# Kernel tuning notes

Hardware: AMD Instinct MI355X
Metric: run time of the kernel (lower is better)

Reference implementation:

```python
import jax, jax.numpy as jnp
import numpy as np
import math

H = 16
D_ATTN = 64
D_MID = 64
D_X = 1024
D_Z = 1024
D_OUT = 1024
B = 2
L_X = 2048
L_Z = 2048
MINUS_INFINITY = -1000000.0

def _xavier(key, shape):
    fan_in, fan_out = shape
    limit = math.sqrt(6.0 / (fan_in + fan_out))
    return jax.random.uniform(key, shape, jnp.float32, -limit, limit)

def setup_inputs() -> dict:
    key = jax.random.key(0)
    ks = jax.random.split(key, 8)
    primary = jax.random.normal(ks[0], (B, L_X, D_X), jnp.float32)
    context = jax.random.normal(ks[1], (B, L_Z, D_Z), jnp.float32)
    padding_mask = jnp.ones((B, L_Z), jnp.int32)
    # causal attention mask (b, l_x, l_z)
    attention_mask = jnp.broadcast_to(
        jnp.tril(jnp.ones((L_X, L_Z), jnp.int32))[None], (B, L_X, L_Z))
    W_qs = _xavier(ks[2], (D_X, H * D_ATTN))
    W_ks = _xavier(ks[3], (D_Z, H * D_ATTN))
    W_vs = _xavier(ks[4], (D_Z, H * D_MID))
    W_o = _xavier(ks[5], (H * D_MID, D_OUT))
    b_o = jnp.zeros((D_OUT,), jnp.float32)
    return {"primary": primary, "context": context,
            "padding_mask": padding_mask, "attention_mask": attention_mask,
            "W_qs": W_qs, "W_ks": W_ks, "W_vs": W_vs, "W_o": W_o, "b_o": b_o}

def reference(primary, context, padding_mask, attention_mask, W_qs, W_ks, W_vs, W_o, b_o):
    b, l_x, _ = primary.shape
    l_z = context.shape[1]
    # QKV projections, split into heads (head-major columns)
    q = (primary @ W_qs).reshape(b, l_x, H, D_ATTN).transpose(0, 2, 1, 3)  # (b,h,l_x,d_attn)
    k = (context @ W_ks).reshape(b, l_z, H, D_ATTN).transpose(0, 2, 1, 3)  # (b,h,l_z,d_attn)
    v = (context @ W_vs).reshape(b, l_z, H, D_MID).transpose(0, 2, 1, 3)   # (b,h,l_z,d_mid)
    scores = jnp.einsum('bhxd,bhzd->bhxz', q, k) / math.sqrt(D_ATTN)
    # combined mask: attention_mask AND padding_mask, broadcast over heads
    mask = (attention_mask * padding_mask[:, None, :])[:, None]  # (b,1,l_x,l_z)
    scores = jnp.where(mask == 0, MINUS_INFINITY, scores)
    attn = jax.nn.softmax(scores, axis=-1)
    out = jnp.einsum('bhxz,bhzm->bhxm', attn, v)  # (b,h,l_x,d_mid)
    out = out.transpose(0, 2, 1, 3).reshape(b, l_x, H * D_MID)
    return out @ W_o + b_o
```

## Files before the change

### kernel.cpp

```cpp
#include <hip/hip_runtime.h>

#define NB 2
#define LX 2048
#define LZ 2048
#define HH 16
#define DA 64
#define DM 64
#define HD 1024
#define KVS 2048
#define MINF  -1000000.0f
#define QSC   0.1803368801f
#define DTHR  8.0f

typedef __attribute__((ext_vector_type(8))) short short8;
typedef __attribute__((ext_vector_type(4))) float f32x4;

static __device__ __forceinline__ ushort f2bf(float f) {
    union { float f; uint32_t u; } c; c.f = f;
    return (ushort)((c.u + 0x7FFFu + ((c.u >> 16) & 1u)) >> 16);
}

static __device__ __forceinline__ float bf2f(ushort u) {
    union { uint32_t u; float f; } c; c.u = (uint32_t)u << 16;
    return c.f;
}

static __device__ __forceinline__ uint32_t cvtpk(float lo, float hi) {
    uint32_t r;
    asm("v_cvt_pk_bf16_f32 %0, %1, %2" : "=v"(r) : "v"(lo), "v"(hi));
    return r;
}

#define GL16(g, l) __builtin_amdgcn_global_load_lds( \
    (const __attribute__((address_space(1))) void*)(g), \
    (__attribute__((address_space(3))) void*)(l), 16, 0, 0)

__global__ __launch_bounds__(256) void prep(
    const float* __restrict__ pA, const float* __restrict__ pB,
    ushort* __restrict__ oA, ushort* __restrict__ oB,
    const float* __restrict__ W0, const float* __restrict__ W1,
    const float* __restrict__ W2, const float* __restrict__ W3,
    ushort* __restrict__ T0, ushort* __restrict__ T1,
    ushort* __restrict__ T2, ushort* __restrict__ T3,
    const int* __restrict__ amask, const int* __restrict__ pmask,
    int* __restrict__ cls)
{
    const int fid = blockIdx.x;
    const int t = threadIdx.x;
    if (fid < 8192) {
        const int i = fid * 256 + t;
        const float* in = (i < 1048576) ? pA : pB;
        ushort* out = (i < 1048576) ? oA : oB;
        const int j = i & 1048575;
        float4 v = ((const float4*)in)[j];
        ushort4 o;
        o.x = f2bf(v.x); o.y = f2bf(v.y); o.z = f2bf(v.z); o.w = f2bf(v.w);
        ((ushort4*)out)[j] = o;
    } else if (fid < 9216) {
        __shared__ ushort Ls[64][72];
        const int id2 = fid - 8192;
        const int zz = id2 >> 8, rem = id2 & 255;
        const float* W = (zz == 0) ? W0 : (zz == 1) ? W1 : (zz == 2) ? W2 : W3;
        ushort* Wt = (zz == 0) ? T0 : (zz == 1) ? T1 : (zz == 2) ? T2 : T3;
        const int n0 = (rem & 15) * 64, k0 = (rem >> 4) * 64;
        const int rr = t >> 4, c4 = (t & 15) * 4;
        #pragma unroll
        for (int i = 0; i < 4; ++i) {
            const int r = rr + i * 16;
            float4 v = *(const float4*)&W[(size_t)(k0 + r) * 1024 + n0 + c4];
            Ls[c4 + 0][r] = f2bf(v.x);
            Ls[c4 + 1][r] = f2bf(v.y);
            Ls[c4 + 2][r] = f2bf(v.z);
            Ls[c4 + 3][r] = f2bf(v.w);
        }
        __syncthreads();
        const int n = t >> 2, kc = (t & 3) * 16;
        *(short8*)&Wt[(size_t)(n0 + n) * 1024 + k0 + kc]     = *(const short8*)&Ls[n][kc];
        *(short8*)&Wt[(size_t)(n0 + n) * 1024 + k0 + kc + 8] = *(const short8*)&Ls[n][kc + 8];
    } else {
        const int bid = fid - 9216;
        const int b = bid >> 10, xb = (bid >> 5) & 31, zb = bid & 31;
        int andv = 1, orv = 0;
        #pragma unroll
        for (int i = 0; i < 16; ++i) {
            const int e = t + i * 256;
            const int r = e >> 6, z = e & 63;
            const int m = amask[((size_t)b * LX + xb * 64 + r) * LZ + zb * 64 + z];
            const int p = pmask[(size_t)b * LZ + zb * 64 + z];
            const int v = (m != 0) & (p != 0);
            andv &= v; orv |= v;
        }
        __shared__ int sa[256];
        __shared__ int so[256];
        sa[t] = andv; so[t] = orv;
        __syncthreads();
        for (int s = 128; s > 0; s >>= 1) {
            if (t < s) { sa[t] &= sa[t + s]; so[t] |= so[t + s]; }
            __syncthreads();
        }
        if (t == 0) cls[bid] = so[0] ? (sa[0] ? 1 : 2) : 0;
    }
}

__global__ __launch_bounds__(256) void gemm_qkv(
    const ushort* __restrict__ Pb, const ushort* __restrict__ Cb,
    const ushort* __restrict__ Wqt, const ushort* __restrict__ Wkvt,
    ushort* __restrict__ Qb, ushort* __restrict__ KV)
{
    const int bx = blockIdx.x;
    const bool isQ = bx < 8;
    const ushort* A  = isQ ? Pb : Cb;
    const ushort* Bt = isQ ? Wqt : Wkvt;
    ushort* Cout = isQ ? Qb : KV;
    const int n0 = (isQ ? bx : bx - 8) * 128;
    const int ostr = isQ ? 1024 : KVS;
    const float osc = isQ ? QSC : 1.0f;

    __shared__ ushort As[128 * 32];
    __shared__ ushort Bs[128 * 32];
    const int t = threadIdx.x;
    const int w = t >> 6, l = t & 63, lr = l & 15, lg = l >> 4;
    const int wr = w >> 1, wc = w & 1;
    const int m0 = blockIdx.y * 128;

    const int c0 = t, c1 = t + 256;
    const ushort* a0 = &A[(size_t)(m0 + (c0 >> 2)) * 1024 + (c0 & 3) * 8];
    const ushort* a1 = &A[(size_t)(m0 + (c1 >> 2)) * 1024 + (c1 & 3) * 8];
    const ushort* b0 = &Bt[(size_t)(n0 + (c0 >> 2)) * 1024 + (c0 & 3) * 8];
    const ushort* b1 = &Bt[(size_t)(n0 + (c1 >> 2)) * 1024 + (c1 & 3) * 8];
    ushort* lA0 = &As[w * 512];
    ushort* lA1 = &As[(4 + w) * 512];
    ushort* lB0 = &Bs[w * 512];
    ushort* lB1 = &Bs[(4 + w) * 512];

    f32x4 acc[4][4];
    #pragma unroll
    for (int i = 0; i < 4; ++i)
        #pragma unroll
        for (int j = 0; j < 4; ++j) acc[i][j] = 0.f;

    for (int k0 = 0; k0 < 1024; k0 += 32) {
        __syncthreads();
        GL16(a0 + k0, lA0);
        GL16(a1 + k0, lA1);
        GL16(b0 + k0, lB0);
        GL16(b1 + k0, lB1);
        __syncthreads();
        short8 af[4], bf[4];
        #pragma unroll
        for (int mi = 0; mi < 4; ++mi)
            af[mi] = *(const short8*)&As[(wr * 64 + mi * 16 + lr) * 32 + lg * 8];
        #pragma unroll
        for (int nj = 0; nj < 4; ++nj)
            bf[nj] = *(const short8*)&Bs[(wc * 64 + nj * 16 + lr) * 32 + lg * 8];
        #pragma unroll
        for (int mi = 0; mi < 4; ++mi)
            #pragma unroll
            for (int nj = 0; nj < 4; ++nj)
                acc[mi][nj] = __builtin_amdgcn_mfma_f32_16x16x32_bf16(
                    af[mi], bf[nj], acc[mi][nj], 0, 0, 0);
    }

    const int row0 = m0 + wr * 64, col0 = n0 + wc * 64;
    #pragma unroll
    for (int mi = 0; mi < 4; ++mi)
        #pragma unroll
        for (int nj = 0; nj < 4; ++nj) {
            const int col = col0 + nj * 16 + lr;
            #pragma unroll
            for (int r = 0; r < 4; ++r) {
                const int row = row0 + mi * 16 + lg * 4 + r;
                Cout[(size_t)row * ostr + col] = f2bf(acc[mi][nj][r] * osc);
            }
        }
}

__global__ __launch_bounds__(256, 4) void attn_mfma(
    const ushort* __restrict__ Qg, const ushort* __restrict__ KVg,
    const int* __restrict__ amask, const int* __restrict__ pmask,
    const int* __restrict__ cls, ushort* __restrict__ Op,
    float2* __restrict__ ml)
{
    __shared__ ushort Ks[64 * 64];
    __shared__ ushort Vt[64 * 64];

    const int t = threadIdx.x, w = t >> 6, l = t & 63, lr = l & 15, lg = l >> 4;
    const int flat = blockIdx.x + 32 * (blockIdx.y + 16 * blockIdx.z);
    const int xcd = flat & 7, ii = flat >> 3;
    const int g = xcd + 8 * (ii >> 5);
    const int xr_ = ii & 31;
    const int h = g & 15, bs = g >> 4;
    const int b = bs & 1, sKV = bs >> 1;
    const int fx = (xr_ & 1) ? 31 - (xr_ >> 1) : (xr_ >> 1);
    const int qb = b ? 31 - fx : fx;
    const int qw = qb * 64 + w * 16;

    short8 qf[2];
    #pragma unroll
    for (int ks = 0; ks < 2; ++ks)
        qf[ks] = *(const short8*)&Qg[(size_t)(b * LX + qw + lr) * HD
                                     + h * DA + ks * 32 + lg * 8];

    float mrun = -1e30f, lrun = 0.f;
    f32x4 o[4];
    #pragma unroll
    for (int mj = 0; mj < 4; ++mj) o[mj] = 0.f;

    const int zs0 = t >> 3, zs1 = 32 + (t >> 3);
    const int cs = t & 7;
    const int gc0 = (cs ^ (zs0 & 7)) << 3;
    ushort* kdst0 = &Ks[w * 512];
    ushort* kdst1 = &Ks[2048 + w * 512];
    const size_t kbase = (size_t)(b * LZ) * KVS + h * DA;

    const int vz = (t >> 3) * 2, vc = (t & 7) * 8;

    for (int zb = sKV; zb < LZ / 64; zb += 2) {
        const int cl = cls[b * 1024 + qb * 32 + zb];
        if (cl == 0) continue;
        const int z0 = zb * 64;

        __syncthreads();
        GL16(&KVg[kbase + (size_t)(z0 + zs0) * KVS + gc0], kdst0);
        GL16(&KVg[kbase + (size_t)(z0 + zs1) * KVS + gc0], kdst1);
        {
            const ushort* vp = &KVg[(size_t)(b * LZ + z0 + vz) * KVS + 1024 + h * DM + vc];
            short8 v0 = *(const short8*)vp;
            short8 v1 = *(const short8*)(vp + KVS);
            const int zc = vz >> 3, zo = vz & 7;
            #pragma unroll
            for (int j = 0; j < 8; ++j) {
                const int m = vc + j;
                const int idx = m * 64 + (((zc ^ m ^ (m >> 3)) & 7) << 3) + zo;
                *(uint32_t*)&Vt[idx] =
                    (uint32_t)(ushort)v0[j] | ((uint32_t)(ushort)v1[j] << 16);
            }
        }
        __syncthreads();

        f32x4 s[4];
        __builtin_amdgcn_s_setprio(1);
        #pragma unroll
        for (int nj = 0; nj < 4; ++nj) {
            const int row = nj * 16 + lr;
            const int sw = row & 7;
            const short8 kf0 = *(const short8*)&Ks[row * 64 + ((lg ^ sw) << 3)];
            const short8 kf1 = *(const short8*)&Ks[row * 64 + (((4 + lg) ^ sw) << 3)];
            f32x4 z4 = 0.f;
            z4 = __builtin_amdgcn_mfma_f32_16x16x32_bf16(kf0, qf[0], z4, 0, 0, 0);
            z4 = __builtin_amdgcn_mfma_f32_16x16x32_bf16(kf1, qf[1], z4, 0, 0, 0);
            s[nj] = z4;
        }
        __builtin_amdgcn_s_setprio(0);
        if (cl == 2) {
            const size_t arow = (size_t)(b * LX + qw + lr) * LZ + z0;
            #pragma unroll
            for (int nj = 0; nj < 4; ++nj)
                #pragma unroll
                for (int r = 0; r < 4; ++r) {
                    const int z = nj * 16 + lg * 4 + r;
                    const int ok = (amask[arow + z] != 0) & (pmask[b * LZ + z0 + z] != 0);
                    if (!ok) s[nj][r] = MINF;
                }
        }
        {
            float pm = s[0][0];
            #pragma unroll
            for (int nj = 0; nj < 4; ++nj)
                #pragma unroll
                for (int r = 0; r < 4; ++r) pm = fmaxf(pm, s[nj][r]);
            pm = fmaxf(pm, __shfl_xor(pm, 16));
            pm = fmaxf(pm, __shfl_xor(pm, 32));
            if (__any(pm > mrun + DTHR)) {
                const float mn = fmaxf(mrun, pm);
                const float al = exp2f(mrun - mn);
                mrun = mn;
                lrun *= al;
                #pragma unroll
                for (int r = 0; r < 4; ++r) {
                    const float alq = __shfl(al, (lg << 2) + r);
                    #pragma unroll
                    for (int mj = 0; mj < 4; ++mj) o[mj][r] *= alq;
                }
            }
            #pragma unroll
            for (int nj = 0; nj < 4; ++nj)
                #pragma unroll
                for (int r = 0; r < 4; ++r) {
                    const float p = exp2f(s[nj][r] - mrun);
                    s[nj][r] = p;
                    lrun += p;
                }
        }
        short8 pa[2];
        {
            uint32_t pk01[4], pk23[4];
            #pragma unroll
            for (int nj = 0; nj < 4; ++nj) {
                pk01[nj] = cvtpk(s[nj][0], s[nj][1]);
                pk23[nj] = cvtpk(s[nj][2], s[nj][3]);
            }
            #pragma unroll
            for (int ks = 0; ks < 2; ++ks) {
                union { uint32_t d[4]; short8 v; } u;
                u.d[0] = pk01[2 * ks];
                u.d[1] = pk23[2 * ks];
                u.d[2] = pk01[2 * ks + 1];
                u.d[3] = pk23[2 * ks + 1];
                pa[ks] = u.v;
            }
        }
        __builtin_amdgcn_s_setprio(1);
        #pragma unroll
        for (int mj = 0; mj < 4; ++mj) {
            const int m_ = mj * 16 + lr;
            const int xr = (m_ ^ (m_ >> 3)) & 7;
            const int czb = lg >> 1;
            const int zo = (lg & 1) * 4;
            #pragma unroll
            for (int ks = 0; ks < 2; ++ks) {
                const int clo = (ks * 4 + czb) ^ xr;
                const int chi = (ks * 4 + 2 + czb) ^ xr;
                const uint2 lo = *(const uint2*)&Vt[m_ * 64 + ((clo & 7) << 3) + zo];
                const uint2 hi = *(const uint2*)&Vt[m_ * 64 + ((chi & 7) << 3) + zo];
                union { uint32_t d[4]; short8 v; } u;
                u.d[0] = lo.x; u.d[1] = lo.y; u.d[2] = hi.x; u.d[3] = hi.y;
                o[mj] = __builtin_amdgcn_mfma_f32_16x16x32_bf16(pa[ks], u.v, o[mj], 0, 0, 0);
            }
        }
        __builtin_amdgcn_s_setprio(0);
    }

    lrun += __shfl_xor(lrun, 16);
    lrun += __shfl_xor(lrun, 32);
    if (l < 16)
        ml[(size_t)((sKV * NB + b) * HH + h) * LX + qw + l] = make_float2(mrun, lrun);
    const size_t ob = (size_t)((sKV * NB + b) * LX + qw) * HD + h * DM;
    #pragma unroll
    for (int r = 0; r < 4; ++r)
        #pragma unroll
        for (int mj = 0; mj < 4; ++mj)
            Op[ob + (size_t)((lg << 2) + r) * HD + mj * 16 + lr] = f2bf(o[mj][r]);
}

__global__ __launch_bounds__(256) void gemm_out_fused(
    const ushort* __restrict__ Op, const float2* __restrict__ ml,
    const ushort* __restrict__ Bt, const float* __restrict__ bias,
    float* __restrict__ Cout)
{
    __shared__ ushort As[64 * 32];
    __shared__ ushort Bs[128 * 32];
    __shared__ float2 Wl[64][17];
    const int t = threadIdx.x;
    const int w = t >> 6, l = t & 63, lr = l & 15, lg = l >> 4;
    const int wr = w >> 1, wc = w & 1;
    const int n0 = blockIdx.x * 128, m0 = blockIdx.y * 64;

    {
        const int e = t * 4;
        #pragma unroll
        for (int j = 0; j < 4; ++j) {
            const int rl = (e + j) >> 4, hh = (e + j) & 15;
            const int ra = m0 + rl;
            const int bb = ra >> 11, xx = ra & 2047;
            const float2 a0 = ml[(size_t)(bb * HH + hh) * LX + xx];
            const float2 a1 = ml[(size_t)((NB + bb) * HH + hh) * LX + xx];
            const float M = fmaxf(a0.x, a1.x);
            const float w0 = exp2f(a0.x - M), w1 = exp2f(a1.x - M);
            const float inv = 1.f / fmaxf(a0.y * w0 + a1.y * w1, 1e-37f);
            Wl[rl][hh] = make_float2(w0 * inv, w1 * inv);
        }
    }
    __syncthreads();

    const int ra = m0 + (t >> 2), ka = (t & 3) * 8;
    const ushort* p0 = &Op[(size_t)ra * HD + ka];
    const ushort* p1 = p0 + (size_t)NB * LX * HD;
    const ushort* b0 = &Bt[(size_t)(n0 + (t >> 2)) * 1024 + ka];
    const ushort* b1 = &Bt[(size_t)(n0 + 64 + (t >> 2)) * 1024 + ka];
    ushort* lB0 = &Bs[w * 512];
    ushort* lB1 = &Bs[(4 + w) * 512];

    f32x4 acc[2][4];
    #pragma unroll
    for (int i = 0; i < 2; ++i)
        #pragma unroll
        for (int j = 0; j < 4; ++j) acc[i][j] = 0.f;

    for (int k0 = 0; k0 < 1024; k0 += 32) {
        const short8 q0 = *(const short8*)(p0 + k0);
        const short8 q1 = *(const short8*)(p1 + k0);
        const float2 wv = Wl[t >> 2][(k0 + ka) >> 6];
        union { ushort d[8]; short8 v; } av;
        #pragma unroll
        for (int j = 0; j < 8; ++j)
            av.d[j] = f2bf(bf2f((ushort)q0[j]) * wv.x + bf2f((ushort)q1[j]) * wv.y);
        __syncthreads();
        *(short8*)&As[t * 8] = av.v;
        GL16(b0 + k0, lB0);
        GL16(b1 + k0, lB1);
        __syncthreads();
        short8 af[2], bf[4];
        #pragma unroll
        for (int mi = 0; mi < 2; ++mi)
            af[mi] = *(const short8*)&As[(wr * 32 + mi * 16 + lr) * 32 + lg * 8];
        #pragma unroll
        for (int nj = 0; nj < 4; ++nj)
            bf[nj] = *(const short8*)&Bs[(wc * 64 + nj * 16 + lr) * 32 + lg * 8];
        #pragma unroll
        for (int mi = 0; mi < 2; ++mi)
            #pragma unroll
            for (int nj = 0; nj < 4; ++nj)
                acc[mi][nj] = __builtin_amdgcn_mfma_f32_16x16x32_bf16(
                    af[mi], bf[nj], acc[mi][nj], 0, 0, 0);
    }

    const int row0 = m0 + wr * 32, col0 = n0 + wc * 64;
    #pragma unroll
    for (int mi = 0; mi < 2; ++mi)
        #pragma unroll
        for (int nj = 0; nj < 4; ++nj) {
            const int col = col0 + nj * 16 + lr;
            #pragma unroll
            for (int r = 0; r < 4; ++r) {
                const int row = row0 + mi * 16 + lg * 4 + r;
                Cout[(size_t)row * 1024 + col] = acc[mi][nj][r] + bias[col];
            }
        }
}

extern "C" void kernel_launch(void* const* d_in, const int* in_sizes, int n_in,
                              void* d_out, int out_size, void* d_ws, size_t ws_size,
                              hipStream_t stream)
{
    const float* primary = (const float*)d_in[0];
    const float* context = (const float*)d_in[1];
    const int*   pmask   = (const int*)d_in[2];
    const int*   amask   = (const int*)d_in[3];
    const float* Wq      = (const float*)d_in[4];
    const float* Wk      = (const float*)d_in[5];
    const float* Wv      = (const float*)d_in[6];
    const float* Wo      = (const float*)d_in[7];
    const float* bo      = (const float*)d_in[8];
    float* out = (float*)d_out;

    char* w8 = (char*)d_ws;
    ushort* Pb  = (ushort*)(w8 + 0);
    ushort* Cb  = (ushort*)(w8 + 8388608);
    ushort* Qb  = (ushort*)(w8 + 16777216);
    ushort* KV  = (ushort*)(w8 + 25165824);
    ushort* Wqt = (ushort*)(w8 + 50331648);
    ushort* Wkt = (ushort*)(w8 + 52428800);
    ushort* Wvt = (ushort*)(w8 + 54525952);
    ushort* Wot = (ushort*)(w8 + 56623104);
    int*    clsp = (int*)(w8 + 58720256);
    ushort* Op   = Pb;
    float2* mlp  = (float2*)Wqt;

    prep<<<11264, 256, 0, stream>>>(primary, context, Pb, Cb,
                                    Wq, Wk, Wv, Wo, Wqt, Wkt, Wvt, Wot,
                                    amask, pmask, clsp);
    gemm_qkv<<<dim3(24, 32), 256, 0, stream>>>(Pb, Cb, Wqt, Wkt, Qb, KV);
    attn_mfma<<<dim3(32, 16, 4), 256, 0, stream>>>(Qb, KV, amask, pmask, clsp, Op, mlp);
    gemm_out_fused<<<dim3(8, 64), 256, 0, stream>>>(Op, mlp, Wot, bo, out);
}
```

Measured before the change: 137.0 us.

## Pair complementary causal query blocks per workgroup to share K/V tile loads

```diff
diff --git a/kernel.cpp b/kernel.cpp
--- a/kernel.cpp
+++ b/kernel.cpp
@@ -185,26 +185,36 @@
     __shared__ ushort Vt[64 * 64];
 
     const int t = threadIdx.x, w = t >> 6, l = t & 63, lr = l & 15, lg = l >> 4;
-    const int flat = blockIdx.x + 32 * (blockIdx.y + 16 * blockIdx.z);
+    const int flat = blockIdx.x + 16 * (blockIdx.y + 16 * blockIdx.z);
     const int xcd = flat & 7, ii = flat >> 3;
-    const int g = xcd + 8 * (ii >> 5);
-    const int xr_ = ii & 31;
+    const int g = xcd + 8 * (ii >> 4);
+    const int pp = ii & 15;
     const int h = g & 15, bs = g >> 4;
     const int b = bs & 1, sKV = bs >> 1;
-    const int fx = (xr_ & 1) ? 31 - (xr_ >> 1) : (xr_ >> 1);
-    const int qb = b ? 31 - fx : fx;
-    const int qw = qb * 64 + w * 16;
-
-    short8 qf[2];
-    #pragma unroll
-    for (int ks = 0; ks < 2; ++ks)
-        qf[ks] = *(const short8*)&Qg[(size_t)(b * LX + qw + lr) * HD
-                                     + h * DA + ks * 32 + lg * 8];
-
-    float mrun = -1e30f, lrun = 0.f;
-    f32x4 o[4];
-    #pragma unroll
-    for (int mj = 0; mj < 4; ++mj) o[mj] = 0.f;
+    const uint32_t halfm = sKV ? 0xAAAAAAAAu : 0x55555555u;
+
+    const int qb0 = pp, qb1 = 31 - pp;
+    const int qw0 = qb0 * 64 + w * 16, qw1 = qb1 * 64 + w * 16;
+    const int cv0 = cls[b * 1024 + qb0 * 32 + (l & 31)];
+    const int cv1 = cls[b * 1024 + qb1 * 32 + (l & 31)];
+    const uint32_t act0 = (uint32_t)__ballot(cv0 != 0) & halfm;
+    const uint32_t mix0 = (uint32_t)__ballot(cv0 == 2) & halfm;
+    const uint32_t act1 = (uint32_t)__ballot(cv1 != 0) & halfm;
+    const uint32_t mix1 = (uint32_t)__ballot(cv1 == 2) & halfm;
+
+    short8 qfA[2], qfB[2];
+    #pragma unroll
+    for (int ks = 0; ks < 2; ++ks) {
+        qfA[ks] = *(const short8*)&Qg[(size_t)(b * LX + qw0 + lr) * HD
+                                      + h * DA + ks * 32 + lg * 8];
+        qfB[ks] = *(const short8*)&Qg[(size_t)(b * LX + qw1 + lr) * HD
+                                      + h * DA + ks * 32 + lg * 8];
+    }
+
+    float mrunA = -1e30f, lrunA = 0.f, mrunB = -1e30f, lrunB = 0.f;
+    f32x4 oA[4], oB[4];
+    #pragma unroll
+    for (int mj = 0; mj < 4; ++mj) { oA[mj] = 0.f; oB[mj] = 0.f; }
 
     const int zs0 = t >> 3, zs1 = 32 + (t >> 3);
     const int cs = t & 7;
@@ -212,12 +222,107 @@
     ushort* kdst0 = &Ks[w * 512];
     ushort* kdst1 = &Ks[2048 + w * 512];
     const size_t kbase = (size_t)(b * LZ) * KVS + h * DA;
-
     const int vz = (t >> 3) * 2, vc = (t & 7) * 8;
 
-    for (int zb = sKV; zb < LZ / 64; zb += 2) {
-        const int cl = cls[b * 1024 + qb * 32 + zb];
-        if (cl == 0) continue;
+#define STRIP_COMPUTE(QW, QF, MRUN, LRUN, OO, MIXBIT)                          \
+    do {                                                                       \
+        f32x4 s[4];                                                           \
+        __builtin_amdgcn_s_setprio(1);                                        \
+        _Pragma("unroll")                                                      \
+        for (int nj = 0; nj < 4; ++nj) {                                      \
+            const int row = nj * 16 + lr;                                     \
+            const int sw = row & 7;                                           \
+            const short8 kf0 = *(const short8*)&Ks[row * 64 + ((lg ^ sw) << 3)];\
+            const short8 kf1 = *(const short8*)&Ks[row * 64 + (((4 + lg) ^ sw) << 3)];\
+            f32x4 z4 = 0.f;                                                   \
+            z4 = __builtin_amdgcn_mfma_f32_16x16x32_bf16(kf0, (QF)[0], z4, 0, 0, 0);\
+            z4 = __builtin_amdgcn_mfma_f32_16x16x32_bf16(kf1, (QF)[1], z4, 0, 0, 0);\
+            s[nj] = z4;                                                       \
+        }                                                                      \
+        __builtin_amdgcn_s_setprio(0);                                        \
+        if (MIXBIT) {                                                          \
+            const size_t arow = (size_t)(b * LX + (QW) + lr) * LZ + z0;       \
+            _Pragma("unroll")                                                  \
+            for (int nj = 0; nj < 4; ++nj)                                    \
+                _Pragma("unroll")                                              \
+                for (int r = 0; r < 4; ++r) {                                 \
+                    const int z = nj * 16 + lg * 4 + r;                       \
+                    const int ok = (amask[arow + z] != 0) & (pmask[b * LZ + z0 + z] != 0);\
+                    if (!ok) s[nj][r] = MINF;                                 \
+                }                                                              \
+        }                                                                      \
+        {                                                                      \
+            float pm = s[0][0];                                               \
+            _Pragma("unroll")                                                  \
+            for (int nj = 0; nj < 4; ++nj)                                    \
+                _Pragma("unroll")                                              \
+                for (int r = 0; r < 4; ++r) pm = fmaxf(pm, s[nj][r]);         \
+            pm = fmaxf(pm, __shfl_xor(pm, 16));                               \
+            pm = fmaxf(pm, __shfl_xor(pm, 32));                               \
+            if (__any(pm > (MRUN) + DTHR)) {                                  \
+                const float mn = fmaxf((MRUN), pm);                           \
+                const float al = exp2f((MRUN) - mn);                          \
+                (MRUN) = mn;                                                  \
+                (LRUN) *= al;                                                 \
+                _Pragma("unroll")                                              \
+                for (int r = 0; r < 4; ++r) {                                 \
+                    const float alq = __shfl(al, (lg << 2) + r);              \
+                    _Pragma("unroll")                                          \
+                    for (int mj = 0; mj < 4; ++mj) (OO)[mj][r] *= alq;        \
+                }                                                              \
+            }                                                                  \
+            _Pragma("unroll")                                                  \
+            for (int nj = 0; nj < 4; ++nj)                                    \
+                _Pragma("unroll")                                              \
+                for (int r = 0; r < 4; ++r) {                                 \
+                    const float p = exp2f(s[nj][r] - (MRUN));                 \
+                    s[nj][r] = p;                                             \
+                    (LRUN) += p;                                              \
+                }                                                              \
+        }                                                                      \
+        short8 pa[2];                                                         \
+        {                                                                      \
+            uint32_t pk01[4], pk23[4];                                        \
+            _Pragma("unroll")                                                  \
+            for (int nj = 0; nj < 4; ++nj) {                                  \
+                pk01[nj] = cvtpk(s[nj][0], s[nj][1]);                         \
+                pk23[nj] = cvtpk(s[nj][2], s[nj][3]);                         \
+            }                                                                  \
+            _Pragma("unroll")                                                  \
+            for (int ks = 0; ks < 2; ++ks) {                                  \
+                union { uint32_t d[4]; short8 v; } u;                         \
+                u.d[0] = pk01[2 * ks];                                        \
+                u.d[1] = pk23[2 * ks];                                        \
+                u.d[2] = pk01[2 * ks + 1];                                    \
+                u.d[3] = pk23[2 * ks + 1];                                    \
+                pa[ks] = u.v;                                                 \
+            }                                                                  \
+        }                                                                      \
+        __builtin_amdgcn_s_setprio(1);                                        \
+        _Pragma("unroll")                                                      \
+        for (int mj = 0; mj < 4; ++mj) {                                      \
+            const int m_ = mj * 16 + lr;                                      \
+            const int xr = (m_ ^ (m_ >> 3)) & 7;                              \
+            const int czb = lg >> 1;                                          \
+            const int zo = (lg & 1) * 4;                                      \
+            _Pragma("unroll")                                                  \
+            for (int ks = 0; ks < 2; ++ks) {                                  \
+                const int clo = (ks * 4 + czb) ^ xr;                          \
+                const int chi = (ks * 4 + 2 + czb) ^ xr;                      \
+                const uint2 lo = *(const uint2*)&Vt[m_ * 64 + ((clo & 7) << 3) + zo];\
+                const uint2 hi = *(const uint2*)&Vt[m_ * 64 + ((chi & 7) << 3) + zo];\
+                union { uint32_t d[4]; short8 v; } u;                         \
+                u.d[0] = lo.x; u.d[1] = lo.y; u.d[2] = hi.x; u.d[3] = hi.y;   \
+                (OO)[mj] = __builtin_amdgcn_mfma_f32_16x16x32_bf16(pa[ks], u.v, (OO)[mj], 0, 0, 0);\
+            }                                                                  \
+        }                                                                      \
+        __builtin_amdgcn_s_setprio(0);                                        \
+    } while (0)
+
+    uint32_t remU = act0 | act1;
+    while (remU) {
+        const int zb = __builtin_ctz(remU);
+        remU &= remU - 1;
         const int z0 = zb * 64;
 
         __syncthreads();
@@ -238,109 +343,30 @@
         }
         __syncthreads();
 
-        f32x4 s[4];
-        __builtin_amdgcn_s_setprio(1);
-        #pragma unroll
-        for (int nj = 0; nj < 4; ++nj) {
-            const int row = nj * 16 + lr;
-            const int sw = row & 7;
-            const short8 kf0 = *(const short8*)&Ks[row * 64 + ((lg ^ sw) << 3)];
-            const short8 kf1 = *(const short8*)&Ks[row * 64 + (((4 + lg) ^ sw) << 3)];
-            f32x4 z4 = 0.f;
-            z4 = __builtin_amdgcn_mfma_f32_16x16x32_bf16(kf0, qf[0], z4, 0, 0, 0);
-            z4 = __builtin_amdgcn_mfma_f32_16x16x32_bf16(kf1, qf[1], z4, 0, 0, 0);
-            s[nj] = z4;
-        }
-        __builtin_amdgcn_s_setprio(0);
-        if (cl == 2) {
-            const size_t arow = (size_t)(b * LX + qw + lr) * LZ + z0;
-            #pragma unroll
-            for (int nj = 0; nj < 4; ++nj)
-                #pragma unroll
-                for (int r = 0; r < 4; ++r) {
-                    const int z = nj * 16 + lg * 4 + r;
-                    const int ok = (amask[arow + z] != 0) & (pmask[b * LZ + z0 + z] != 0);
-                    if (!ok) s[nj][r] = MINF;
-                }
-        }
-        {
-            float pm = s[0][0];
-            #pragma unroll
-            for (int nj = 0; nj < 4; ++nj)
-                #pragma unroll
-                for (int r = 0; r < 4; ++r) pm = fmaxf(pm, s[nj][r]);
-            pm = fmaxf(pm, __shfl_xor(pm, 16));
-            pm = fmaxf(pm, __shfl_xor(pm, 32));
-            if (__any(pm > mrun + DTHR)) {
-                const float mn = fmaxf(mrun, pm);
-                const float al = exp2f(mrun - mn);
-                mrun = mn;
-                lrun *= al;
-                #pragma unroll
-                for (int r = 0; r < 4; ++r) {
-                    const float alq = __shfl(al, (lg << 2) + r);
-                    #pragma unroll
-                    for (int mj = 0; mj < 4; ++mj) o[mj][r] *= alq;
-                }
-            }
-            #pragma unroll
-            for (int nj = 0; nj < 4; ++nj)
-                #pragma unroll
-                for (int r = 0; r < 4; ++r) {
-                    const float p = exp2f(s[nj][r] - mrun);
-                    s[nj][r] = p;
-                    lrun += p;
-                }
-        }
-        short8 pa[2];
-        {
-            uint32_t pk01[4], pk23[4];
-            #pragma unroll
-            for (int nj = 0; nj < 4; ++nj) {
-                pk01[nj] = cvtpk(s[nj][0], s[nj][1]);
-                pk23[nj] = cvtpk(s[nj][2], s[nj][3]);
-            }
-            #pragma unroll
-            for (int ks = 0; ks < 2; ++ks) {
-                union { uint32_t d[4]; short8 v; } u;
-                u.d[0] = pk01[2 * ks];
-                u.d[1] = pk23[2 * ks];
-                u.d[2] = pk01[2 * ks + 1];
-                u.d[3] = pk23[2 * ks + 1];
-                pa[ks] = u.v;
-            }
-        }
-        __builtin_amdgcn_s_setprio(1);
+        if ((act0 >> zb) & 1)
+            STRIP_COMPUTE(qw0, qfA, mrunA, lrunA, (&oA[0] - 0), ((mix0 >> zb) & 1));
+        if ((act1 >> zb) & 1)
+            STRIP_COMPUTE(qw1, qfB, mrunB, lrunB, (&oB[0] - 0), ((mix1 >> zb) & 1));
+    }
+#undef STRIP_COMPUTE
+
+    lrunA += __shfl_xor(lrunA, 16);
+    lrunA += __shfl_xor(lrunA, 32);
+    lrunB += __shfl_xor(lrunB, 16);
+    lrunB += __shfl_xor(lrunB, 32);
+    if (l < 16) {
+        ml[(size_t)((sKV * NB + b) * HH + h) * LX + qw0 + l] = make_float2(mrunA, lrunA);
+        ml[(size_t)((sKV * NB + b) * HH + h) * LX + qw1 + l] = make_float2(mrunB, lrunB);
+    }
+    const size_t ob0 = (size_t)((sKV * NB + b) * LX + qw0) * HD + h * DM;
+    const size_t ob1 = (size_t)((sKV * NB + b) * LX + qw1) * HD + h * DM;
+    #pragma unroll
+    for (int r = 0; r < 4; ++r)
         #pragma unroll
         for (int mj = 0; mj < 4; ++mj) {
-            const int m_ = mj * 16 + lr;
-            const int xr = (m_ ^ (m_ >> 3)) & 7;
-            const int czb = lg >> 1;
-            const int zo = (lg & 1) * 4;
-            #pragma unroll
-            for (int ks = 0; ks < 2; ++ks) {
-                const int clo = (ks * 4 + czb) ^ xr;
-                const int chi = (ks * 4 + 2 + czb) ^ xr;
-                const uint2 lo = *(const uint2*)&Vt[m_ * 64 + ((clo & 7) << 3) + zo];
-                const uint2 hi = *(const uint2*)&Vt[m_ * 64 + ((chi & 7) << 3) + zo];
-                union { uint32_t d[4]; short8 v; } u;
-                u.d[0] = lo.x; u.d[1] = lo.y; u.d[2] = hi.x; u.d[3] = hi.y;
-                o[mj] = __builtin_amdgcn_mfma_f32_16x16x32_bf16(pa[ks], u.v, o[mj], 0, 0, 0);
-            }
-        }
-        __builtin_amdgcn_s_setprio(0);
-    }
-
-    lrun += __shfl_xor(lrun, 16);
-    lrun += __shfl_xor(lrun, 32);
-    if (l < 16)
-        ml[(size_t)((sKV * NB + b) * HH + h) * LX + qw + l] = make_float2(mrun, lrun);
-    const size_t ob = (size_t)((sKV * NB + b) * LX + qw) * HD + h * DM;
-    #pragma unroll
-    for (int r = 0; r < 4; ++r)
-        #pragma unroll
-        for (int mj = 0; mj < 4; ++mj)
-            Op[ob + (size_t)((lg << 2) + r) * HD + mj * 16 + lr] = f2bf(o[mj][r]);
+            Op[ob0 + (size_t)((lg << 2) + r) * HD + mj * 16 + lr] = f2bf(oA[mj][r]);
+            Op[ob1 + (size_t)((lg << 2) + r) * HD + mj * 16 + lr] = f2bf(oB[mj][r]);
+        }
 }
 
 __global__ __launch_bounds__(256) void gemm_out_fused(
@@ -461,6 +487,6 @@
                                     Wq, Wk, Wv, Wo, Wqt, Wkt, Wvt, Wot,
                                     amask, pmask, clsp);
     gemm_qkv<<<dim3(24, 32), 256, 0, stream>>>(Pb, Cb, Wqt, Wkt, Qb, KV);
-    attn_mfma<<<dim3(32, 16, 4), 256, 0, stream>>>(Qb, KV, amask, pmask, clsp, Op, mlp);
+    attn_mfma<<<dim3(16, 16, 4), 256, 0, stream>>>(Qb, KV, amask, pmask, clsp, Op, mlp);
     gemm_out_fused<<<dim3(8, 64), 256, 0, stream>>>(Op, mlp, Wot, bo, out);
 }
```

Result: faster. 131.6 us, median of 3 (-3.9%).
